# Kernel optimization log

Measured on AMD Instinct MI355X. Metric: run time of the kernel, lower is better.

## Reference

```python
import jax, jax.numpy as jnp
import numpy as np

N_NODES = 100000
N_EDGES = 3200000
N_GRAPHS = 3200

def setup_inputs() -> dict:
    key = jax.random.key(0)
    ks = jax.random.split(key, 12)
    def glorot(k, shape):
        lim = np.sqrt(6.0 / (shape[0] + shape[1]))
        return jax.random.uniform(k, shape, jnp.float32, -lim, lim)
    x = jax.random.normal(ks[0], (N_NODES, 37), jnp.float32)
    edge_index = jax.random.randint(ks[1], (2, N_EDGES), 0, N_NODES, jnp.int64 if jax.config.jax_enable_x64 else jnp.int32)
    batch = jnp.sort(jax.random.randint(ks[2], (N_NODES,), 0, N_GRAPHS))
    return {
        'x': x,
        'W1': glorot(ks[3], (37, 128)),  'b1': jnp.zeros((128,), jnp.float32),
        'W2': glorot(ks[4], (128, 256)), 'b2': jnp.zeros((256,), jnp.float32),
        'W3': glorot(ks[5], (256, 256)), 'b3': jnp.zeros((256,), jnp.float32),
        'Wp': glorot(ks[6], (256, 256)), 'bp': jnp.zeros((256,), jnp.float32),
        'edge_index': edge_index,
        'batch': batch,
    }

def _gcn_conv(h, W, b, src, dst, dis):
    # PyG GCNConv: h' = D^{-1/2}(A+I)D^{-1/2} (h W) + b, self-loops added
    hW = h @ W
    norm = dis[src] * dis[dst]                      # [E]
    msg = hW[src] * norm[:, None]                   # gather + scale
    agg = jax.ops.segment_sum(msg, dst, num_segments=N_NODES)
    agg = agg + hW * (dis * dis)[:, None]           # self-loop contribution
    return agg + b

def reference(x, W1, b1, W2, b2, W3, b3, Wp, bp, edge_index, batch):
    src, dst = edge_index[0], edge_index[1]
    # degree with self-loops (all edge weights = 1)
    deg = jax.ops.segment_sum(jnp.ones((N_EDGES,), x.dtype), dst, num_segments=N_NODES) + 1.0
    dis = jax.lax.rsqrt(deg)
    h = jax.nn.relu(_gcn_conv(x, W1, b1, src, dst, dis))
    h = jax.nn.relu(_gcn_conv(h, W2, b2, src, dst, dis))
    h = jax.nn.relu(_gcn_conv(h, W3, b3, src, dst, dis))
    # global mean pool over graphs
    sums = jax.ops.segment_sum(h, batch, num_segments=N_GRAPHS)
    cnts = jax.ops.segment_sum(jnp.ones((N_NODES,), x.dtype), batch, num_segments=N_GRAPHS)
    pooled = sums / jnp.maximum(cnts, 1.0)[:, None]
    return pooled @ Wp + bp
```

## Files before the change

### kernel.cpp

```cpp
#include <hip/hip_runtime.h>

#define N_NODES  100000
#define N_EDGES  3200000
#define N_GRAPHS 3200

#define NBLK 200
#define EB   16000
#define BSH  7
#define NB   ((N_NODES + 127) >> BSH)
#define BCAP 5120

typedef __attribute__((ext_vector_type(8))) short bf16x8;
typedef __attribute__((ext_vector_type(4))) float f32x4;

__device__ __forceinline__ float bf2f(unsigned short u) {
    return __uint_as_float(((unsigned)u) << 16);
}
__device__ __forceinline__ unsigned short f2bf(float f) {
    unsigned u = __float_as_uint(f);
    u += 0x7fffu + ((u >> 16) & 1u);
    return (unsigned short)(u >> 16);
}


__global__ __launch_bounds__(256, 4)
void hist_kernel(const int* __restrict__ dst, int* __restrict__ hist) {
    __shared__ int lh[NB];
    int blk = blockIdx.x, t = threadIdx.x;
    for (int b = t; b < NB; b += 256) lh[b] = 0;
    __syncthreads();
    int e0 = blk * EB;
    for (int i = t; i < EB; i += 256)
        atomicAdd(&lh[dst[e0 + i] >> BSH], 1);
    __syncthreads();
    for (int b = t; b < NB; b += 256) hist[b * NBLK + blk] = lh[b];
}

__global__ void bucket_tot_kernel(const int* __restrict__ hist, int* __restrict__ tot) {
    int b = blockIdx.x, l = threadIdx.x;
    int s = 0;
    for (int k = l; k < NBLK; k += 64) s += hist[b * NBLK + k];
    for (int off = 32; off; off >>= 1) s += __shfl_down(s, off);
    if (l == 0) tot[b] = s;
}

__global__ void bucket_scan_kernel(const int* __restrict__ tot, int* __restrict__ bucketStart) {
    __shared__ int part[256];
    int t = threadIdx.x;
    int chunk = (NB + 255) / 256;
    int lo = t * chunk; if (lo > NB) lo = NB;
    int hi = lo + chunk; if (hi > NB) hi = NB;
    int s = 0;
    for (int i = lo; i < hi; ++i) s += tot[i];
    part[t] = s;
    __syncthreads();
    for (int off = 1; off < 256; off <<= 1) {
        int v = part[t];
        int a = (t >= off) ? part[t - off] : 0;
        __syncthreads();
        part[t] = v + a;
        __syncthreads();
    }
    int run = (t == 0) ? 0 : part[t - 1];
    for (int i = lo; i < hi; ++i) { bucketStart[i] = run; run += tot[i]; }
    if (t == 255) bucketStart[NB] = run;
}

__global__ void bucket_base_kernel(int* __restrict__ hist, const int* __restrict__ bucketStart) {
    int b = blockIdx.x * blockDim.x + threadIdx.x;
    if (b >= NB) return;
    int run = bucketStart[b];
    int* row = hist + b * NBLK;
#pragma unroll 4
    for (int k = 0; k < NBLK; ++k) { int v = row[k]; row[k] = run; run += v; }
}

__global__ __launch_bounds__(256, 4)
void scatter1_kernel(const int* __restrict__ src, const int* __restrict__ dst,
                     const int* __restrict__ base, int* __restrict__ spk) {
    __shared__ int lcur[NB];
    int blk = blockIdx.x, t = threadIdx.x;
    for (int b = t; b < NB; b += 256) lcur[b] = base[b * NBLK + blk];
    __syncthreads();
    int e0 = blk * EB;
    for (int i = t; i < EB; i += 256) {
        int d = dst[e0 + i], s = src[e0 + i];
        int pos = atomicAdd(&lcur[d >> BSH], 1);
        spk[pos] = ((d & 127) << 17) | s;
    }
}

__global__ __launch_bounds__(256, 1)
void csr2_kernel(const int* __restrict__ spk,
                 const int* __restrict__ bucketStart,
                 int* __restrict__ offsets, float* __restrict__ dis,
                 int* __restrict__ csr_src) {
    __shared__ int lpk[BCAP];
    __shared__ int lhist[128], loff[128], lcur[128];
    int b = blockIdx.x, t = threadIdx.x;
    int n0 = b << BSH;
    int e0 = bucketStart[b], e1 = bucketStart[b + 1];
    int cnt = e1 - e0; if (cnt > BCAP) cnt = BCAP;
    for (int i = t; i < cnt; i += 256) lpk[i] = spk[e0 + i];
    if (t < 128) lhist[t] = 0;
    __syncthreads();
    for (int i = t; i < cnt; i += 256) atomicAdd(&lhist[lpk[i] >> 17], 1);
    __syncthreads();
    if (t < 128) loff[t] = lhist[t];
    __syncthreads();
    for (int off = 1; off < 128; off <<= 1) {
        int v = 0;
        if (t < 128) { v = loff[t]; if (t >= off) v += loff[t - off]; }
        __syncthreads();
        if (t < 128) loff[t] = v;
        __syncthreads();
    }
    if (t < 128) {
        int excl = loff[t] - lhist[t];
        lcur[t] = excl;
        int n = n0 + t;
        if (n < N_NODES) {
            offsets[n] = e0 + excl;
            dis[n] = rsqrtf((float)lhist[t] + 1.0f);
        }
    }
    if (b == 0 && t == 0) offsets[N_NODES] = N_EDGES;
    __syncthreads();
    for (int i = t; i < cnt; i += 256) {
        int v = lpk[i];
        int pos = atomicAdd(&lcur[v >> 17], 1);
        csr_src[e0 + pos] = v & 0x1FFFF;
    }
}

template<int K, int N>
__global__ void pack_w_kernel(const float* __restrict__ W, int Krows,
                              unsigned short* __restrict__ hi,
                              unsigned short* __restrict__ lo) {
    constexpr int KS = K / 32;
    int idx = blockIdx.x * blockDim.x + threadIdx.x;
    if (idx >= (N / 16) * KS * 64) return;
    int l = idx & 63;
    int s = (idx >> 6) % KS;
    int t = idx / (64 * KS);
    int k0 = s * 32 + (l >> 4) * 8;
    int n  = t * 16 + (l & 15);
    size_t base = (size_t)idx * 8;
#pragma unroll
    for (int j = 0; j < 8; ++j) {
        int k = k0 + j;
        float w = (k < Krows) ? W[(size_t)k * N + n] : 0.0f;
        unsigned short h = f2bf(w);
        float rem = w - bf2f(h);
        hi[base + j] = h;
        lo[base + j] = f2bf(rem);
    }
}

__global__ __launch_bounds__(256, 4)
void cast_x_kernel(const float* __restrict__ x, const float* __restrict__ dis,
                   unsigned short* __restrict__ xb) {
    int idx = blockIdx.x * blockDim.x + threadIdx.x;
    if (idx >= N_NODES * 64) return;
    int n = idx >> 6, c = idx & 63;
    xb[idx] = (c < 37) ? f2bf(x[(size_t)n * 37 + c] * dis[n]) : (unsigned short)0;
}

template<int F>
__device__ __forceinline__ void agg_range(const unsigned short* __restrict__ tab,
                                          const int* __restrict__ csr_src,
                                          int j, int hi, int lane, float* acc) {
    for (; j + 16 <= hi; j += 16) {
        int sidx[16];
#pragma unroll
        for (int u = 0; u < 16; ++u) sidx[u] = csr_src[j + u];
        if (F == 64) {
            unsigned short v[16];
#pragma unroll
            for (int u = 0; u < 16; ++u) v[u] = tab[(size_t)sidx[u] * 64 + lane];
#pragma unroll
            for (int u = 0; u < 16; ++u) acc[0] += bf2f(v[u]);
        } else if (F == 128) {
            ushort2 v[16];
#pragma unroll
            for (int u = 0; u < 16; ++u)
                v[u] = ((const ushort2*)(tab + (size_t)sidx[u] * F))[lane];
#pragma unroll
            for (int u = 0; u < 16; ++u) { acc[0] += bf2f(v[u].x); acc[1] += bf2f(v[u].y); }
        } else {
            ushort4 v[16];
#pragma unroll
            for (int u = 0; u < 16; ++u)
                v[u] = ((const ushort4*)(tab + (size_t)sidx[u] * F))[lane];
#pragma unroll
            for (int u = 0; u < 16; ++u) {
                acc[0] += bf2f(v[u].x); acc[1] += bf2f(v[u].y);
                acc[2] += bf2f(v[u].z); acc[3] += bf2f(v[u].w);
            }
        }
    }
    for (; j + 4 <= hi; j += 4) {
        int sidx[4];
#pragma unroll
        for (int u = 0; u < 4; ++u) sidx[u] = csr_src[j + u];
        if (F == 64) {
            unsigned short v[4];
#pragma unroll
            for (int u = 0; u < 4; ++u) v[u] = tab[(size_t)sidx[u] * 64 + lane];
#pragma unroll
            for (int u = 0; u < 4; ++u) acc[0] += bf2f(v[u]);
        } else if (F == 128) {
            ushort2 v[4];
#pragma unroll
            for (int u = 0; u < 4; ++u)
                v[u] = ((const ushort2*)(tab + (size_t)sidx[u] * F))[lane];
#pragma unroll
            for (int u = 0; u < 4; ++u) { acc[0] += bf2f(v[u].x); acc[1] += bf2f(v[u].y); }
        } else {
            ushort4 v[4];
#pragma unroll
            for (int u = 0; u < 4; ++u)
                v[u] = ((const ushort4*)(tab + (size_t)sidx[u] * F))[lane];
#pragma unroll
            for (int u = 0; u < 4; ++u) {
                acc[0] += bf2f(v[u].x); acc[1] += bf2f(v[u].y);
                acc[2] += bf2f(v[u].z); acc[3] += bf2f(v[u].w);
            }
        }
    }
    for (; j < hi; ++j) {
        int s = csr_src[j];
        if (F == 64) {
            acc[0] += bf2f(tab[(size_t)s * 64 + lane]);
        } else if (F == 128) {
            ushort2 u = ((const ushort2*)(tab + (size_t)s * F))[lane];
            acc[0] += bf2f(u.x); acc[1] += bf2f(u.y);
        } else {
            ushort4 u = ((const ushort4*)(tab + (size_t)s * F))[lane];
            acc[0] += bf2f(u.x); acc[1] += bf2f(u.y); acc[2] += bf2f(u.z); acc[3] += bf2f(u.w);
        }
    }
}

template<int K, int NTW, int N, int MODE>
__global__ __launch_bounds__(256, 8)
void fused_agg_gemm(const unsigned short* __restrict__ tab,
                    const int* __restrict__ csr_src,
                    const int* __restrict__ offsets,
                    const float* __restrict__ dis,
                    const unsigned short* __restrict__ Bhi,
                    const unsigned short* __restrict__ Blo,
                    const float* __restrict__ bias,
                    unsigned short* __restrict__ out) {
    constexpr int KS = K / 32;
    __shared__ unsigned short ldsA[32 * K];
    char* lb = (char*)ldsA;
    int l = threadIdx.x & 63;
    int w = threadIdx.x >> 6;
    int m0 = blockIdx.x * 32;

    for (int i = 0; i < 8; ++i) {
        int r = w * 8 + i;
        int n = m0 + r;
        float acc[(K + 63) / 64];
        if (K == 64) {
            acc[0] = bf2f(tab[(size_t)n * 64 + l]);
        } else if (K == 128) {
            ushort2 u = ((const ushort2*)(tab + (size_t)n * K))[l];
            acc[0] = bf2f(u.x); acc[1] = bf2f(u.y);
        } else {
            ushort4 u = ((const ushort4*)(tab + (size_t)n * K))[l];
            acc[0] = bf2f(u.x); acc[1] = bf2f(u.y); acc[2] = bf2f(u.z); acc[3] = bf2f(u.w);
        }
        agg_range<K>(tab, csr_src, offsets[n], offsets[n + 1], l, acc);
        float d = dis[n];
        unsigned sw = (unsigned)((r & 7) << 4);
        if (K == 64) {
            *(unsigned short*)(lb + ((unsigned)(r * 128 + l * 2) ^ sw)) = f2bf(d * acc[0]);
        } else if (K == 128) {
            ushort2 o; o.x = f2bf(d * acc[0]); o.y = f2bf(d * acc[1]);
            *(ushort2*)(lb + ((unsigned)(r * 256 + l * 4) ^ sw)) = o;
        } else {
            ushort4 o;
            o.x = f2bf(d * acc[0]); o.y = f2bf(d * acc[1]);
            o.z = f2bf(d * acc[2]); o.w = f2bf(d * acc[3]);
            *(ushort4*)(lb + ((unsigned)(r * 512 + l * 8) ^ sw)) = o;
        }
    }
    __syncthreads();

    int n0 = w * (NTW * 16);
    f32x4 acc0[NTW], acc1[NTW];
#pragma unroll
    for (int tn = 0; tn < NTW; ++tn) { acc0[tn] = (f32x4){0,0,0,0}; acc1[tn] = (f32x4){0,0,0,0}; }

    int r0 = l & 15, r1 = r0 + 16;
    unsigned sw0 = (unsigned)((r0 & 7) << 4);
#pragma unroll
    for (int s = 0; s < KS; ++s) {
        unsigned kb = (unsigned)(s * 64 + (l >> 4) * 16);
        bf16x8 af0 = *(const bf16x8*)(lb + ((unsigned)(r0 * K * 2 + kb) ^ sw0));
        bf16x8 af1 = *(const bf16x8*)(lb + ((unsigned)(r1 * K * 2 + kb) ^ sw0));
#pragma unroll
        for (int tn = 0; tn < NTW; ++tn) {
            int t = (n0 >> 4) + tn;
            size_t boff = ((size_t)(t * KS + s) * 64 + l) * 8;
            bf16x8 bh = *(const bf16x8*)(Bhi + boff);
            bf16x8 bl = *(const bf16x8*)(Blo + boff);
            acc0[tn] = __builtin_amdgcn_mfma_f32_16x16x32_bf16(af0, bh, acc0[tn], 0, 0, 0);
            acc0[tn] = __builtin_amdgcn_mfma_f32_16x16x32_bf16(af0, bl, acc0[tn], 0, 0, 0);
            acc1[tn] = __builtin_amdgcn_mfma_f32_16x16x32_bf16(af1, bh, acc1[tn], 0, 0, 0);
            acc1[tn] = __builtin_amdgcn_mfma_f32_16x16x32_bf16(af1, bl, acc1[tn], 0, 0, 0);
        }
    }

    int rowg = (l >> 4) * 4;
#pragma unroll
    for (int tn = 0; tn < NTW; ++tn) {
        int n = n0 + tn * 16 + (l & 15);
        float b = bias[n];
#pragma unroll
        for (int r = 0; r < 4; ++r) {
#pragma unroll
            for (int half = 0; half < 2; ++half) {
                int m = m0 + half * 16 + rowg + r;
                float v = fmaxf((half ? acc1[tn][r] : acc0[tn][r]) + b, 0.0f);
                if (MODE == 1) out[(size_t)m * N + n] = f2bf(v * dis[m]);
                else           out[(size_t)m * N + n] = f2bf(v);
            }
        }
    }
}

__device__ __forceinline__ int lower_bound_dev(const int* __restrict__ a, int n, int key) {
    int lo = 0, hi = n;
    while (lo < hi) {
        int mid = (lo + hi) >> 1;
        if (a[mid] < key) lo = mid + 1; else hi = mid;
    }
    return lo;
}

__global__ __launch_bounds__(256, 4)
void pool_bf16_kernel(const unsigned short* __restrict__ h, const int* __restrict__ batch,
                      float* __restrict__ pooled) {
    int wave = threadIdx.x >> 6;
    int lane = threadIdx.x & 63;
    int g = blockIdx.x * 4 + wave;
    int lo = lower_bound_dev(batch, N_NODES, g);
    int hi = lower_bound_dev(batch, N_NODES, g + 1);
    float a0 = 0, a1 = 0, a2 = 0, a3 = 0;
    for (int n = lo; n < hi; ++n) {
        ushort4 u = ((const ushort4*)(h + (size_t)n * 256))[lane];
        a0 += bf2f(u.x); a1 += bf2f(u.y); a2 += bf2f(u.z); a3 += bf2f(u.w);
    }
    float inv = 1.0f / fmaxf((float)(hi - lo), 1.0f);
    float4 o = {a0 * inv, a1 * inv, a2 * inv, a3 * inv};
    *(float4*)&pooled[(size_t)g * 256 + lane * 4] = o;
}

__global__ __launch_bounds__(256, 2)
void head_gemm_kernel(const float* __restrict__ H, const float* __restrict__ W,
                      const float* __restrict__ bias, float* __restrict__ out) {
    __shared__ float lds[16 * 256];
    int row0 = blockIdx.x * 16;
    int t = threadIdx.x;
    const float* src = H + (size_t)row0 * 256;
    for (int i = t; i < 16 * 256; i += 256) lds[i] = src[i];
    __syncthreads();
    float acc[16];
#pragma unroll
    for (int r = 0; r < 16; ++r) acc[r] = 0.0f;
#pragma unroll 4
    for (int k = 0; k < 256; ++k) {
        float wv = W[k * 256 + t];
#pragma unroll
        for (int r = 0; r < 16; ++r) acc[r] += lds[r * 256 + k] * wv;
    }
#pragma unroll
    for (int r = 0; r < 16; ++r)
        out[(size_t)(row0 + r) * 256 + t] = acc[r] + bias[t];
}

static inline size_t align_up(size_t x, size_t a) { return (x + a - 1) & ~(a - 1); }

extern "C" void kernel_launch(void* const* d_in, const int* in_sizes, int n_in,
                              void* d_out, int out_size, void* d_ws, size_t ws_size,
                              hipStream_t stream) {
    const float* x  = (const float*)d_in[0];
    const float* W1 = (const float*)d_in[1];
    const float* b1 = (const float*)d_in[2];
    const float* W2 = (const float*)d_in[3];
    const float* b2 = (const float*)d_in[4];
    const float* W3 = (const float*)d_in[5];
    const float* b3 = (const float*)d_in[6];
    const float* Wp = (const float*)d_in[7];
    const float* bp = (const float*)d_in[8];
    const int*   ei = (const int*)d_in[9];
    const int*   batch = (const int*)d_in[10];
    float* out = (float*)d_out;

    const int* e_src = ei;
    const int* e_dst = ei + N_EDGES;

    char* p = (char*)d_ws;
    size_t off = 0;
    auto take = [&](size_t bytes) {
        void* r = p + off;
        off = align_up(off + bytes, 256);
        return r;
    };
    int*   hist        = (int*)  take(sizeof(int) * NB * NBLK);
    int*   tot         = (int*)  take(sizeof(int) * NB);
    int*   bucketStart = (int*)  take(sizeof(int) * (NB + 1));
    int*   offsets     = (int*)  take(sizeof(int) * (N_NODES + 1));
    int*   csr_src     = (int*)  take(sizeof(int) * N_EDGES);
    float* dis         = (float*)take(sizeof(float) * N_NODES);
    float* pooled      = (float*)take(sizeof(float) * N_GRAPHS * 256);
    unsigned short* whi1 = (unsigned short*)take(sizeof(unsigned short) * 64 * 128);
    unsigned short* wlo1 = (unsigned short*)take(sizeof(unsigned short) * 64 * 128);
    unsigned short* whi2 = (unsigned short*)take(sizeof(unsigned short) * 128 * 256);
    unsigned short* wlo2 = (unsigned short*)take(sizeof(unsigned short) * 128 * 256);
    unsigned short* whi3 = (unsigned short*)take(sizeof(unsigned short) * 256 * 256);
    unsigned short* wlo3 = (unsigned short*)take(sizeof(unsigned short) * 256 * 256);
    unsigned short* bufX = (unsigned short*)take(sizeof(unsigned short) * (size_t)N_NODES * 256);
    unsigned short* bufY = (unsigned short*)take(sizeof(unsigned short) * (size_t)N_NODES * 256);
    unsigned short* h3   = (unsigned short*)take(sizeof(unsigned short) * (size_t)N_NODES * 256);

    int* spk = (int*)h3;

    unsigned short* xb     = bufY;
    unsigned short* table2 = bufX;
    unsigned short* table3 = bufY;

    hist_kernel<<<NBLK, 256, 0, stream>>>(e_dst, hist);
    bucket_tot_kernel<<<NB, 64, 0, stream>>>(hist, tot);
    bucket_scan_kernel<<<1, 256, 0, stream>>>(tot, bucketStart);
    bucket_base_kernel<<<(NB + 255) / 256, 256, 0, stream>>>(hist, bucketStart);
    scatter1_kernel<<<NBLK, 256, 0, stream>>>(e_src, e_dst, hist, spk);
    csr2_kernel<<<NB, 256, 0, stream>>>(spk, bucketStart, offsets, dis, csr_src);

    pack_w_kernel<64, 128><<<((128 / 16) * 2 * 64 + 255) / 256, 256, 0, stream>>>(W1, 37, whi1, wlo1);
    pack_w_kernel<128, 256><<<((256 / 16) * 4 * 64 + 255) / 256, 256, 0, stream>>>(W2, 128, whi2, wlo2);
    pack_w_kernel<256, 256><<<((256 / 16) * 8 * 64 + 255) / 256, 256, 0, stream>>>(W3, 256, whi3, wlo3);

    cast_x_kernel<<<(N_NODES * 64 + 255) / 256, 256, 0, stream>>>(x, dis, xb);
    fused_agg_gemm<64, 2, 128, 1><<<N_NODES / 32, 256, 0, stream>>>(
        xb, csr_src, offsets, dis, whi1, wlo1, b1, table2);

    fused_agg_gemm<128, 4, 256, 1><<<N_NODES / 32, 256, 0, stream>>>(
        table2, csr_src, offsets, dis, whi2, wlo2, b2, table3);

    fused_agg_gemm<256, 4, 256, 2><<<N_NODES / 32, 256, 0, stream>>>(
        table3, csr_src, offsets, dis, whi3, wlo3, b3, h3);

    pool_bf16_kernel<<<N_GRAPHS / 4, 256, 0, stream>>>(h3, batch, pooled);
    head_gemm_kernel<<<N_GRAPHS / 16, 256, 0, stream>>>(pooled, Wp, bp, out);
}
```

Measured before the change: 625.1 us.

## Sort each node's CSR neighbors by source-ID tile and store per-tile offsets

The CSR build now buckets each destination node's incoming edges by source-ID range (8192-node tiles), so the gather in the aggregation kernels visits sources in roughly ascending order for better cache locality. It writes a per-node table of 14 tile offsets instead of a single offsets array, but the aggregation kernels read only the first and last entries. This adds a much larger offsets array (N*14 ints) to write and read, plus more shared-memory histogram work in csr2.

```diff
diff --git a/kernel.cpp b/kernel.cpp
--- a/kernel.cpp
+++ b/kernel.cpp
@@ -9,6 +9,9 @@
 #define BSH  7
 #define NB   ((N_NODES + 127) >> BSH)
 #define BCAP 5120
+#define TSH2 13
+#define NT2  13
+#define TST  14
 
 typedef __attribute__((ext_vector_type(8))) short bf16x8;
 typedef __attribute__((ext_vector_type(4))) float f32x4;
@@ -93,20 +96,30 @@
 __global__ __launch_bounds__(256, 1)
 void csr2_kernel(const int* __restrict__ spk,
                  const int* __restrict__ bucketStart,
-                 int* __restrict__ offsets, float* __restrict__ dis,
+                 int* __restrict__ tileoff, float* __restrict__ dis,
                  int* __restrict__ csr_src) {
     __shared__ int lpk[BCAP];
-    __shared__ int lhist[128], loff[128], lcur[128];
+    __shared__ int lh[128 * TST];
+    __shared__ int loff[128], ldeg[128];
     int b = blockIdx.x, t = threadIdx.x;
     int n0 = b << BSH;
     int e0 = bucketStart[b], e1 = bucketStart[b + 1];
     int cnt = e1 - e0; if (cnt > BCAP) cnt = BCAP;
     for (int i = t; i < cnt; i += 256) lpk[i] = spk[e0 + i];
-    if (t < 128) lhist[t] = 0;
-    __syncthreads();
-    for (int i = t; i < cnt; i += 256) atomicAdd(&lhist[lpk[i] >> 17], 1);
-    __syncthreads();
-    if (t < 128) loff[t] = lhist[t];
+    for (int i = t; i < 128 * TST; i += 256) lh[i] = 0;
+    __syncthreads();
+    for (int i = t; i < cnt; i += 256) {
+        int v = lpk[i];
+        atomicAdd(&lh[(v >> 17) * TST + ((v & 0x1FFFF) >> TSH2)], 1);
+    }
+    __syncthreads();
+    if (t < 128) {
+        int run = 0;
+#pragma unroll
+        for (int p = 0; p < NT2; ++p) { int v = lh[t * TST + p]; lh[t * TST + p] = run; run += v; }
+        ldeg[t] = run;
+        loff[t] = run;
+    }
     __syncthreads();
     for (int off = 1; off < 128; off <<= 1) {
         int v = 0;
@@ -116,20 +129,28 @@
         __syncthreads();
     }
     if (t < 128) {
-        int excl = loff[t] - lhist[t];
-        lcur[t] = excl;
+        int excl = loff[t] - ldeg[t];
         int n = n0 + t;
         if (n < N_NODES) {
-            offsets[n] = e0 + excl;
-            dis[n] = rsqrtf((float)lhist[t] + 1.0f);
-        }
-    }
-    if (b == 0 && t == 0) offsets[N_NODES] = N_EDGES;
+#pragma unroll
+            for (int p = 0; p < NT2; ++p) {
+                int v = lh[t * TST + p] + excl;
+                lh[t * TST + p] = v;
+                tileoff[(size_t)n * TST + p] = e0 + v;
+            }
+            tileoff[(size_t)n * TST + NT2] = e0 + excl + ldeg[t];
+            dis[n] = rsqrtf((float)ldeg[t] + 1.0f);
+        } else {
+#pragma unroll
+            for (int p = 0; p < NT2; ++p) lh[t * TST + p] += excl;
+        }
+    }
     __syncthreads();
     for (int i = t; i < cnt; i += 256) {
         int v = lpk[i];
-        int pos = atomicAdd(&lcur[v >> 17], 1);
-        csr_src[e0 + pos] = v & 0x1FFFF;
+        int s = v & 0x1FFFF;
+        int pos = atomicAdd(&lh[(v >> 17) * TST + (s >> TSH2)], 1);
+        csr_src[e0 + pos] = s;
     }
 }
 
@@ -246,7 +267,7 @@
 __global__ __launch_bounds__(256, 8)
 void fused_agg_gemm(const unsigned short* __restrict__ tab,
                     const int* __restrict__ csr_src,
-                    const int* __restrict__ offsets,
+                    const int* __restrict__ tileoff,
                     const float* __restrict__ dis,
                     const unsigned short* __restrict__ Bhi,
                     const unsigned short* __restrict__ Blo,
@@ -272,7 +293,9 @@
             ushort4 u = ((const ushort4*)(tab + (size_t)n * K))[l];
             acc[0] = bf2f(u.x); acc[1] = bf2f(u.y); acc[2] = bf2f(u.z); acc[3] = bf2f(u.w);
         }
-        agg_range<K>(tab, csr_src, offsets[n], offsets[n + 1], l, acc);
+        int lo = tileoff[(size_t)n * TST + 0];
+        int hi = tileoff[(size_t)n * TST + NT2];
+        agg_range<K>(tab, csr_src, lo, hi, l, acc);
         float d = dis[n];
         unsigned sw = (unsigned)((r & 7) << 4);
         if (K == 64) {
@@ -413,7 +436,7 @@
     int*   hist        = (int*)  take(sizeof(int) * NB * NBLK);
     int*   tot         = (int*)  take(sizeof(int) * NB);
     int*   bucketStart = (int*)  take(sizeof(int) * (NB + 1));
-    int*   offsets     = (int*)  take(sizeof(int) * (N_NODES + 1));
+    int*   tileoff     = (int*)  take(sizeof(int) * (size_t)N_NODES * TST);
     int*   csr_src     = (int*)  take(sizeof(int) * N_EDGES);
     float* dis         = (float*)take(sizeof(float) * N_NODES);
     float* pooled      = (float*)take(sizeof(float) * N_GRAPHS * 256);
@@ -438,7 +461,7 @@
     bucket_scan_kernel<<<1, 256, 0, stream>>>(tot, bucketStart);
     bucket_base_kernel<<<(NB + 255) / 256, 256, 0, stream>>>(hist, bucketStart);
     scatter1_kernel<<<NBLK, 256, 0, stream>>>(e_src, e_dst, hist, spk);
-    csr2_kernel<<<NB, 256, 0, stream>>>(spk, bucketStart, offsets, dis, csr_src);
+    csr2_kernel<<<NB, 256, 0, stream>>>(spk, bucketStart, tileoff, dis, csr_src);
 
     pack_w_kernel<64, 128><<<((128 / 16) * 2 * 64 + 255) / 256, 256, 0, stream>>>(W1, 37, whi1, wlo1);
     pack_w_kernel<128, 256><<<((256 / 16) * 4 * 64 + 255) / 256, 256, 0, stream>>>(W2, 128, whi2, wlo2);
@@ -446,13 +469,13 @@
 
     cast_x_kernel<<<(N_NODES * 64 + 255) / 256, 256, 0, stream>>>(x, dis, xb);
     fused_agg_gemm<64, 2, 128, 1><<<N_NODES / 32, 256, 0, stream>>>(
-        xb, csr_src, offsets, dis, whi1, wlo1, b1, table2);
+        xb, csr_src, tileoff, dis, whi1, wlo1, b1, table2);
 
     fused_agg_gemm<128, 4, 256, 1><<<N_NODES / 32, 256, 0, stream>>>(
-        table2, csr_src, offsets, dis, whi2, wlo2, b2, table3);
+        table2, csr_src, tileoff, dis, whi2, wlo2, b2, table3);
 
     fused_agg_gemm<256, 4, 256, 2><<<N_NODES / 32, 256, 0, stream>>>(
-        table3, csr_src, offsets, dis, whi3, wlo3, b3, h3);
+        table3, csr_src, tileoff, dis, whi3, wlo3, b3, h3);
 
     pool_bf16_kernel<<<N_GRAPHS / 4, 256, 0, stream>>>(h3, batch, pooled);
     head_gemm_kernel<<<N_GRAPHS / 16, 256, 0, stream>>>(pooled, Wp, bp, out);
```

Measured after the change: 631.9 us. About the same (+1.1%).
